# Optimization experiments

Measured on AMD Instinct MI355X. Metric: run time of the kernel, lower is better.

## Reference

```python
import jax, jax.numpy as jnp
import numpy as np

B, N, C = 32, 512, 256          # batch, proposals per scene, pooled feature dim
K = 16                          # knn neighbors
NN = B * N                      # total nodes = 16384
E = NN * K                      # total edges = 262144
L0_IN = 2 * C + 7               # EdgeConv layer-0 input (edge embedding appended)
EPS = 1e-5


def _xavier(key, fan_in, fan_out):
    s = float(np.sqrt(6.0 / (fan_in + fan_out)))
    return jax.random.uniform(key, (fan_in, fan_out), jnp.float32, -s, s)


def setup_inputs() -> dict:
    key = jax.random.key(0)
    ks = jax.random.split(key, 12)
    inp = {}
    inp["pooled_features"] = jax.random.normal(ks[0], (B, N, C), jnp.float32)
    inp["rois"] = jax.random.normal(ks[1], (B, N, 7), jnp.float32)
    inp["edge_src"] = jax.random.randint(ks[2], (E,), 0, NN)
    inp["edge_dst"] = jax.random.randint(ks[3], (E,), 0, NN)
    # global-info MLP: Linear(C+7 -> C) + BatchNorm(C) + ReLU
    inp["Wg"] = _xavier(ks[4], C + 7, C)
    inp["bg"] = jnp.zeros((C,), jnp.float32)
    inp["gg"] = jnp.ones((C,), jnp.float32)
    inp["betag"] = jnp.zeros((C,), jnp.float32)
    # EdgeConv 0: Linear(2C+7 -> C); EdgeConv 1,2: Linear(2C -> C)
    inp["W0"] = _xavier(ks[5], L0_IN, C)
    inp["b0"] = jnp.zeros((C,), jnp.float32)
    inp["g0"] = jnp.ones((C,), jnp.float32)
    inp["beta0"] = jnp.zeros((C,), jnp.float32)
    inp["W1"] = _xavier(ks[6], 2 * C, C)
    inp["b1"] = jnp.zeros((C,), jnp.float32)
    inp["g1"] = jnp.ones((C,), jnp.float32)
    inp["beta1"] = jnp.zeros((C,), jnp.float32)
    inp["W2"] = _xavier(ks[7], 2 * C, C)
    inp["b2"] = jnp.zeros((C,), jnp.float32)
    inp["g2"] = jnp.ones((C,), jnp.float32)
    inp["beta2"] = jnp.zeros((C,), jnp.float32)
    return inp


def _bn_relu(h, gamma, beta):
    # training-mode BatchNorm over the row (node/edge) dimension
    mu = jnp.mean(h, axis=0)
    var = jnp.mean(jnp.square(h - mu), axis=0)
    return jax.nn.relu((h - mu) * jax.lax.rsqrt(var + EPS) * gamma + beta)


def _edge_conv(x, src, dst, edge_attr, W, b, gamma, beta):
    x_j = x[src]          # source-node features  [E, D]
    x_i = x[dst]          # target-node features  [E, D]
    parts = [x_j - x_i, x_i]
    if edge_attr is not None:
        parts.append(edge_attr)
    m = jnp.concatenate(parts, axis=-1)          # [E, in_dim]
    h = _bn_relu(m @ W + b, gamma, beta)         # [E, C]
    out = jax.ops.segment_max(h, dst, num_segments=NN)  # scatter-max per target node
    return jnp.where(jnp.isneginf(out), 0.0, out)        # empty segments -> 0


def reference(pooled_features, rois, edge_src, edge_dst,
              Wg, bg, gg, betag,
              W0, b0, g0, beta0,
              W1, b1, g1, beta1,
              W2, b2, g2, beta2):
    boxes = rois.reshape(NN, 7)
    pf = pooled_features.reshape(NN, C)
    # global information MLP (CONCATENATED): cat(pooled, boxes) -> Linear+BN+ReLU
    x0 = _bn_relu(jnp.concatenate([pf, boxes], axis=-1) @ Wg + bg, gg, betag)
    # edge embedding: box delta from source to target
    edge_attr = boxes[edge_src] - boxes[edge_dst]
    x1 = _edge_conv(x0, edge_src, edge_dst, edge_attr, W0, b0, g0, beta0)
    x2 = _edge_conv(x1, edge_src, edge_dst, None, W1, b1, g1, beta1)
    x3 = _edge_conv(x2, edge_src, edge_dst, None, W2, b2, g2, beta2)
    return jnp.concatenate([x0, x1, x2, x3], axis=-1)  # related_features [NN, 4C]
```

## Files before the change

kernel.cpp:

```cpp
#include <hip/hip_runtime.h>
#include <hip/hip_bf16.h>
#include <hip/hip_fp16.h>
#include <math.h>
#include <stdint.h>


constexpr int NNODE = 16384;
constexpr int NEDGE = 262144;
constexpr int CD    = 256;
constexpr float EPSB = 1e-5f;

typedef __attribute__((ext_vector_type(8))) short bf16x8;
typedef __attribute__((ext_vector_type(8))) unsigned short u16x8;
typedef __attribute__((ext_vector_type(4))) float f32x4;
typedef __attribute__((ext_vector_type(4))) _Float16 h16x4;
typedef __attribute__((ext_vector_type(8))) _Float16 h16x8;

__device__ inline unsigned short bf_hi_rne(float f) {
  unsigned int u = __float_as_uint(f);
  u += 0x7fffu + ((u >> 16) & 1u);
  return (unsigned short)(u >> 16);
}

__device__ __forceinline__ void gload16(const void* g, void* l) {
  __builtin_amdgcn_global_load_lds(
      (__attribute__((address_space(1))) void*)(void*)g,
      (__attribute__((address_space(3))) void*)l, 16, 0, 0);
}

__global__ void build_wt(const float* __restrict__ W, const float* __restrict__ b,
                         unsigned short* __restrict__ Wth, unsigned short* __restrict__ Wtl,
                         int has_box) {
  int k = threadIdx.x;
  int n = blockIdx.x;
  if (k >= 288) return;
  float v = 0.0f;
  if (n < 256) {
    if (k < 256)      v = W[k * 256 + n];
    else if (k < 263) v = has_box ? W[(512 + (k - 256)) * 256 + n] : 0.0f;
  } else {
    int n2 = n - 256;
    if (k < 256)      v = W[(256 + k) * 256 + n2] - W[k * 256 + n2];
    else if (k < 263) v = has_box ? -W[(512 + (k - 256)) * 256 + n2] : 0.0f;
    else if (k == 263) v = b[n2];
  }
  unsigned short hi = bf_hi_rne(v);
  float fh = __uint_as_float((unsigned int)hi << 16);
  Wth[n * 288 + k] = hi;
  Wtl[n * 288 + k] = bf_hi_rne(v - fh);
}

__global__ void build_wtg(const float* __restrict__ Wg, const float* __restrict__ bg,
                          unsigned short* __restrict__ Wth, unsigned short* __restrict__ Wtl) {
  int k = threadIdx.x;
  int n = blockIdx.x;
  if (k >= 288) return;
  float v = 0.0f;
  if (k < 263)       v = Wg[k * 256 + n];
  else if (k == 263) v = bg[n];
  unsigned short hi = bf_hi_rne(v);
  float fh = __uint_as_float((unsigned int)hi << 16);
  Wth[n * 288 + k] = hi;
  Wtl[n * 288 + k] = bf_hi_rne(v - fh);
}

__global__ void build_boxf16(const float* __restrict__ rois,
                             unsigned short* __restrict__ hi, unsigned short* __restrict__ lo) {
  int n = blockIdx.x * 256 + threadIdx.x;
  u16x8 h8 = (u16x8)0, l8 = (u16x8)0;
#pragma unroll
  for (int j = 0; j < 8; j++) {
    float v = (j < 7) ? rois[n * 7 + j] : 1.0f;
    unsigned short h = bf_hi_rne(v);
    h8[j] = h;
    l8[j] = bf_hi_rne(v - __uint_as_float((unsigned int)h << 16));
  }
  *(u16x8*)(hi + (size_t)n * 32) = h8;
  *(u16x8*)(lo + (size_t)n * 32) = l8;
  u16x8 z = (u16x8)0;
#pragma unroll
  for (int c = 1; c < 4; c++) {
    *(u16x8*)(hi + (size_t)n * 32 + c * 8) = z;
    *(u16x8*)(lo + (size_t)n * 32 + c * 8) = z;
  }
}

__global__ void convert_split(const float* __restrict__ src,
                              unsigned short* __restrict__ hi, unsigned short* __restrict__ lo) {
  size_t i0 = ((size_t)blockIdx.x * 256 + threadIdx.x) * 8;
  float4 a = *(const float4*)(src + i0);
  float4 b = *(const float4*)(src + i0 + 4);
  float v[8] = {a.x, a.y, a.z, a.w, b.x, b.y, b.z, b.w};
  u16x8 h8, l8;
#pragma unroll
  for (int j = 0; j < 8; j++) {
    unsigned short h = bf_hi_rne(v[j]);
    h8[j] = h;
    l8[j] = bf_hi_rne(v[j] - __uint_as_float((unsigned int)h << 16));
  }
  *(u16x8*)(hi + i0) = h8;
  *(u16x8*)(lo + i0) = l8;
}

__global__ void hist_kernel(const int* __restrict__ dst, int* __restrict__ counts) {
  int e = blockIdx.x * 256 + threadIdx.x;
  atomicAdd(&counts[dst[e]], 1);
}

__global__ __launch_bounds__(1024) void scan_kernel(const int* __restrict__ counts,
                                                    int* __restrict__ offsets,
                                                    int* __restrict__ cursor) {
  __shared__ int ssum[1024];
  int t = threadIdx.x;
  int base = t * 16;
  int loc[16];
  int s = 0;
#pragma unroll
  for (int i = 0; i < 16; i++) { loc[i] = s; s += counts[base + i]; }
  ssum[t] = s;
  __syncthreads();
  for (int off = 1; off < 1024; off <<= 1) {
    int v = (t >= off) ? ssum[t - off] : 0;
    __syncthreads();
    ssum[t] += v;
    __syncthreads();
  }
  int excl = (t > 0) ? ssum[t - 1] : 0;
#pragma unroll
  for (int i = 0; i < 16; i++) {
    int o = excl + loc[i];
    offsets[base + i] = o;
    cursor[base + i]  = o;
  }
  if (t == 1023) offsets[NNODE] = excl + s;
}

__global__ void scatter_kernel(const int* __restrict__ src, const int* __restrict__ dst,
                               int* __restrict__ cursor, int* __restrict__ csr_src) {
  int e = blockIdx.x * 256 + threadIdx.x;
  int p = atomicAdd(&cursor[dst[e]], 1);
  csr_src[p] = src[e];
}

__global__ __launch_bounds__(256) void gemm_mfma(
    const unsigned short* __restrict__ Ah, const unsigned short* __restrict__ Al,
    const unsigned short* __restrict__ bxh, const unsigned short* __restrict__ bxl,
    const unsigned short* __restrict__ Wth, const unsigned short* __restrict__ Wtl,
    float* __restrict__ out, int Nw, int half_out) {
  __shared__ alignas(16) char lds[4 * 8192];
  const int tid  = threadIdx.x;
  const int lane = tid & 63;
  const int wave = tid >> 6;
  const int wm = wave >> 1, wn = wave & 1;
  const int m0 = blockIdx.x * 128;
  const int n0 = blockIdx.y * 128;
  const int srow = tid >> 2;
  const int sc8  = (tid & 3) * 8;

  f32x4 acc[4][4];
#pragma unroll
  for (int i = 0; i < 4; i++)
#pragma unroll
    for (int j = 0; j < 4; j++) acc[i][j] = (f32x4)0.0f;

  const int kblk = lane >> 4;
  for (int kt = 0; kt < 9; kt++) {
    if (kt) __syncthreads();
#pragma unroll
    for (int p = 0; p < 2; p++) {
      int row = p * 64 + srow;
      const unsigned short *gah, *gal;
      if (kt < 8) {
        size_t o = (size_t)(m0 + row) * 256 + kt * 32 + sc8;
        gah = Ah + o; gal = Al + o;
      } else {
        size_t o = (size_t)(m0 + row) * 32 + sc8;
        gah = bxh + o; gal = bxl + o;
      }
      gload16(gah, lds + p * 4096 + tid * 16);
      gload16(gal, lds + 8192 + p * 4096 + tid * 16);
      size_t wo = (size_t)(n0 + row) * 288 + kt * 32 + sc8;
      gload16(Wth + wo, lds + 16384 + p * 4096 + tid * 16);
      gload16(Wtl + wo, lds + 24576 + p * 4096 + tid * 16);
    }
    __syncthreads();

    bf16x8 ah[4], al[4];
#pragma unroll
    for (int i = 0; i < 4; i++) {
      int fm = wm * 64 + i * 16 + (lane & 15);
      int off = fm * 64 + 16 * kblk;
      ah[i] = *(const bf16x8*)(lds + off);
      al[i] = *(const bf16x8*)(lds + 8192 + off);
    }
#pragma unroll
    for (int j = 0; j < 4; j++) {
      int fn = wn * 64 + j * 16 + (lane & 15);
      int off = fn * 64 + 16 * kblk;
      bf16x8 bh = *(const bf16x8*)(lds + 16384 + off);
      bf16x8 bl = *(const bf16x8*)(lds + 24576 + off);
#pragma unroll
      for (int i = 0; i < 4; i++) {
        acc[i][j] = __builtin_amdgcn_mfma_f32_16x16x32_bf16(bh, ah[i], acc[i][j], 0, 0, 0);
        acc[i][j] = __builtin_amdgcn_mfma_f32_16x16x32_bf16(bh, al[i], acc[i][j], 0, 0, 0);
        acc[i][j] = __builtin_amdgcn_mfma_f32_16x16x32_bf16(bl, ah[i], acc[i][j], 0, 0, 0);
      }
    }
  }
#pragma unroll
  for (int i = 0; i < 4; i++) {
    int m = m0 + wm * 64 + i * 16 + (lane & 15);
#pragma unroll
    for (int j = 0; j < 4; j++) {
      int n = n0 + wn * 64 + j * 16 + (lane >> 4) * 4;
      if (half_out) {
        h16x4 o;
        o[0] = (_Float16)acc[i][j].x; o[1] = (_Float16)acc[i][j].y;
        o[2] = (_Float16)acc[i][j].z; o[3] = (_Float16)acc[i][j].w;
        *(h16x4*)((_Float16*)out + (size_t)m * Nw + n) = o;
      } else {
        *(f32x4*)(out + (size_t)m * Nw + n) = acc[i][j];
      }
    }
  }
}

constexpr int EPB = 8;
__global__ __launch_bounds__(256) void edge_pass(
    const _Float16* __restrict__ PQ,
    const int* __restrict__ offsets, const int* __restrict__ csr_src,
    float* __restrict__ M, float* __restrict__ psum, float* __restrict__ psq) {
  __shared__ float red[2][4][256];
  const int tid = threadIdx.x;
  const int wave = tid >> 6, lane = tid & 63;
  const int h = lane >> 5, li = lane & 31;
  const int c8 = li * 8;
  float sum[8] = {}, sq[8] = {};

  const int d0 = blockIdx.x * EPB + wave * 2;
  const int d1 = d0 + 1;
  int e0 = offsets[d0];
  const int end0 = offsets[d0 + 1];
  int e1 = offsets[d1];
  const int end1 = offsets[d1 + 1];

  h16x8 q0v = *(const h16x8*)(PQ + (size_t)d0 * 512 + 256 + c8);
  h16x8 q1v = *(const h16x8*)(PQ + (size_t)d1 * 512 + 256 + c8);
  float q0[8], q1[8], mx0[8], mx1[8];
#pragma unroll
  for (int j = 0; j < 8; j++) {
    q0[j] = (float)q0v[j]; q1[j] = (float)q1v[j];
    mx0[j] = -INFINITY;    mx1[j] = -INFINITY;
  }

  while (e0 < end0 || e1 < end1) {
    const bool a0 = e0 < end0, a1 = e1 < end1;
    int i0[4], i1[4];
    if (a0) {
#pragma unroll
      for (int i = 0; i < 4; i++) {
        int ei = e0 + 2 * i + h;
        i0[i] = csr_src[ei < end0 ? ei : end0 - 1];
      }
    }
    if (a1) {
#pragma unroll
      for (int i = 0; i < 4; i++) {
        int ei = e1 + 2 * i + h;
        i1[i] = csr_src[ei < end1 ? ei : end1 - 1];
      }
    }
    h16x8 p0[4], p1[4];
    if (a0) {
#pragma unroll
      for (int i = 0; i < 4; i++)
        p0[i] = *(const h16x8*)(PQ + (size_t)i0[i] * 512 + c8);
    }
    if (a1) {
#pragma unroll
      for (int i = 0; i < 4; i++)
        p1[i] = *(const h16x8*)(PQ + (size_t)i1[i] * 512 + c8);
    }

#define PROC_NODE(P, Q, MX, EE, END)                                        \
    {                                                                       \
      const int nl = (END) - (EE);                                          \
      if (nl >= 8) {                                                        \
        _Pragma("unroll")                                                   \
        for (int i = 0; i < 4; i++)                                         \
          _Pragma("unroll")                                                 \
          for (int j = 0; j < 8; j++) {                                     \
            float hh = (float)P[i][j] + Q[j];                               \
            MX[j] = fmaxf(MX[j], hh);                                       \
            sum[j] += hh; sq[j] = fmaf(hh, hh, sq[j]);                      \
          }                                                                 \
      } else {                                                              \
        _Pragma("unroll")                                                   \
        for (int i = 0; i < 4; i++) {                                       \
          const bool live = (2 * i + h) < nl;                               \
          _Pragma("unroll")                                                 \
          for (int j = 0; j < 8; j++) {                                     \
            float hh = (float)P[i][j] + Q[j];                               \
            MX[j] = fmaxf(MX[j], hh);                                       \
            float z = live ? hh : 0.f;                                      \
            sum[j] += z; sq[j] = fmaf(z, z, sq[j]);                         \
          }                                                                 \
        }                                                                   \
      }                                                                     \
    }

    if (a0) { PROC_NODE(p0, q0, mx0, e0, end0); e0 += 8; }
    if (a1) { PROC_NODE(p1, q1, mx1, e1, end1); e1 += 8; }
#undef PROC_NODE
  }

#pragma unroll
  for (int j = 0; j < 8; j++) {
    mx0[j] = fmaxf(mx0[j], __shfl_xor(mx0[j], 32));
    mx1[j] = fmaxf(mx1[j], __shfl_xor(mx1[j], 32));
  }
  float4 o0 = (h == 0) ? make_float4(mx0[0], mx0[1], mx0[2], mx0[3])
                       : make_float4(mx0[4], mx0[5], mx0[6], mx0[7]);
  float4 o1 = (h == 0) ? make_float4(mx1[0], mx1[1], mx1[2], mx1[3])
                       : make_float4(mx1[4], mx1[5], mx1[6], mx1[7]);
  *(float4*)(M + (size_t)d0 * 256 + c8 + h * 4) = o0;
  *(float4*)(M + (size_t)d1 * 256 + c8 + h * 4) = o1;

#pragma unroll
  for (int j = 0; j < 8; j++) {
    sum[j] += __shfl_xor(sum[j], 32);
    sq[j]  += __shfl_xor(sq[j], 32);
  }
  if (h == 0) {
    *(float4*)&red[0][wave][c8]     = make_float4(sum[0], sum[1], sum[2], sum[3]);
    *(float4*)&red[0][wave][c8 + 4] = make_float4(sum[4], sum[5], sum[6], sum[7]);
    *(float4*)&red[1][wave][c8]     = make_float4(sq[0], sq[1], sq[2], sq[3]);
    *(float4*)&red[1][wave][c8 + 4] = make_float4(sq[4], sq[5], sq[6], sq[7]);
  }
  __syncthreads();
  int c = tid;
  float ts = red[0][0][c] + red[0][1][c] + red[0][2][c] + red[0][3][c];
  float tq = red[1][0][c] + red[1][1][c] + red[1][2][c] + red[1][3][c];
  atomicAdd(&psum[c], ts);
  atomicAdd(&psq[c], tq);
}

__global__ void stats_dense(const float* __restrict__ H,
                            float* __restrict__ psum, float* __restrict__ psq) {
  int c  = threadIdx.x;
  int r0 = blockIdx.x * 16;
  float sum = 0.f, sq = 0.f;
  for (int r = r0; r < r0 + 16; r++) {
    float h = H[r * CD + c];
    sum += h;
    sq  += h * h;
  }
  atomicAdd(&psum[c], sum);
  atomicAdd(&psq[c], sq);
}

__global__ void finalize_stats(const float* __restrict__ psum, const float* __restrict__ psq,
                               float invcount, float* __restrict__ mu, float* __restrict__ rstd) {
  int c = threadIdx.x;
  float m = psum[c] * invcount;
  float v = psq[c] * invcount - m * m;
  v = fmaxf(v, 0.0f);
  mu[c]   = m;
  rstd[c] = 1.0f / sqrtf(v + EPSB);
}

__global__ void normalize_write(const float* __restrict__ H, const int* __restrict__ counts,
                                const float* __restrict__ mu, const float* __restrict__ rstd,
                                const float* __restrict__ gamma, const float* __restrict__ beta,
                                float* __restrict__ out, int col0,
                                unsigned short* __restrict__ xh, unsigned short* __restrict__ xl) {
  int c  = threadIdx.x;
  int n0 = blockIdx.x * 8;
  float mc = mu[c], rc = rstd[c], gc = gamma[c], bc = beta[c];
  for (int n = n0; n < n0 + 8; n++) {
    float v = 0.0f;
    if (!counts || counts[n] != 0) {
      float h = H[n * CD + c];
      v = fmaxf((h - mc) * rc * gc + bc, 0.0f);
    }
    out[n * 1024 + col0 + c] = v;
    if (xh) {
      unsigned short hv = bf_hi_rne(v);
      xh[(size_t)n * 256 + c] = hv;
      xl[(size_t)n * 256 + c] = bf_hi_rne(v - __uint_as_float((unsigned int)hv << 16));
    }
  }
}

extern "C" void kernel_launch(void* const* d_in, const int* in_sizes, int n_in,
                              void* d_out, int out_size, void* d_ws, size_t ws_size,
                              hipStream_t stream) {
  const float* pf    = (const float*)d_in[0];
  const float* rois  = (const float*)d_in[1];
  const int*   esrc  = (const int*)d_in[2];
  const int*   edst  = (const int*)d_in[3];
  const float* Wg    = (const float*)d_in[4];
  const float* bg    = (const float*)d_in[5];
  const float* gg    = (const float*)d_in[6];
  const float* betag = (const float*)d_in[7];
  const float* Wl[3]  = {(const float*)d_in[8],  (const float*)d_in[12], (const float*)d_in[16]};
  const float* bl[3]  = {(const float*)d_in[9],  (const float*)d_in[13], (const float*)d_in[17]};
  const float* gl[3]  = {(const float*)d_in[10], (const float*)d_in[14], (const float*)d_in[18]};
  const float* bel[3] = {(const float*)d_in[11], (const float*)d_in[15], (const float*)d_in[19]};
  float* out = (float*)d_out;

  float* ws    = (float*)d_ws;
  _Float16* PQ = (_Float16*)ws;
  float* Mbuf  = ws + (size_t)NNODE * 256;
  float* psum  = Mbuf + (size_t)NNODE * CD;
  float* psq   = psum + CD;
  float* mu    = psq + CD;
  float* rstd  = mu + CD;
  unsigned short* Ah = (unsigned short*)(rstd + CD);
  unsigned short* Al = Ah + (size_t)NNODE * 256;
  unsigned short* bxh = Al + (size_t)NNODE * 256;
  unsigned short* bxl = bxh + (size_t)NNODE * 32;
  unsigned short* wt  = bxl + (size_t)NNODE * 32;
  unsigned short* wtg_h = wt + 3 * 2 * 512 * 288;
  unsigned short* wtg_l = wtg_h + 256 * 288;
  int* counts  = (int*)(wtg_l + 256 * 288);
  int* offsets = counts + NNODE;
  int* cursor  = offsets + NNODE + 1;
  int* csr     = cursor + NNODE;

  hipMemsetAsync(counts, 0, NNODE * sizeof(int), stream);
  build_boxf16<<<NNODE / 256, 256, 0, stream>>>(rois, bxh, bxl);
  convert_split<<<NNODE * CD / (256 * 8), 256, 0, stream>>>(pf, Ah, Al);
  build_wtg<<<256, 320, 0, stream>>>(Wg, bg, wtg_h, wtg_l);
  for (int l = 0; l < 3; l++)
    build_wt<<<512, 320, 0, stream>>>(Wl[l], bl[l],
                                      wt + l * 2 * 512 * 288,
                                      wt + l * 2 * 512 * 288 + 512 * 288,
                                      l == 0 ? 1 : 0);
  hist_kernel<<<NEDGE / 256, 256, 0, stream>>>(edst, counts);
  scan_kernel<<<1, 1024, 0, stream>>>(counts, offsets, cursor);
  scatter_kernel<<<NEDGE / 256, 256, 0, stream>>>(esrc, edst, cursor, csr);

  hipMemsetAsync(psum, 0, 2 * CD * sizeof(float), stream);
  {
    dim3 g(NNODE / 128, 2);
    gemm_mfma<<<g, 256, 0, stream>>>(Ah, Al, bxh, bxl, wtg_h, wtg_l, Mbuf, 256, 0);
  }
  stats_dense<<<NNODE / 16, 256, 0, stream>>>(Mbuf, psum, psq);
  finalize_stats<<<1, 256, 0, stream>>>(psum, psq, 1.0f / NNODE, mu, rstd);
  normalize_write<<<NNODE / 8, 256, 0, stream>>>(Mbuf, nullptr, mu, rstd, gg, betag,
                                                 out, 0, Ah, Al);

  for (int l = 0; l < 3; l++) {
    dim3 g(NNODE / 128, 4);
    gemm_mfma<<<g, 256, 0, stream>>>(Ah, Al, bxh, bxl,
                                     wt + l * 2 * 512 * 288,
                                     wt + l * 2 * 512 * 288 + 512 * 288,
                                     (float*)PQ, 512, 1);
    hipMemsetAsync(psum, 0, 2 * CD * sizeof(float), stream);
    edge_pass<<<NNODE / EPB, 256, 0, stream>>>(PQ, offsets, csr, Mbuf, psum, psq);
    finalize_stats<<<1, 256, 0, stream>>>(psum, psq, 1.0f / NEDGE, mu, rstd);
    normalize_write<<<NNODE / 8, 256, 0, stream>>>(Mbuf, counts, mu, rstd, gl[l], bel[l],
                                                   out, (l + 1) * CD,
                                                   l < 2 ? Ah : nullptr,
                                                   l < 2 ? Al : nullptr);
  }
}
```

Measured before the change: 495.2 us.

## Drop split-bf16 error compensation and restructure edge pass with fp16 packed math

Removes the hi/lo bf16 split for activations, boxes and weights, so each GEMM issues one MFMA per tile instead of three and loads half as much data into half the LDS. The edge pass now assigns one destination node per wave in 512-thread blocks, double-buffers the neighbour gathers, skips empty nodes, and computes add and max in packed fp16. Accuracy drops to plain bf16 GEMM inputs and fp16 intermediate sums, which may breach the tolerance against the fp32 reference.

```diff
diff --git a/kernel.cpp b/kernel.cpp
--- a/kernel.cpp
+++ b/kernel.cpp
@@ -15,6 +15,7 @@
 typedef __attribute__((ext_vector_type(4))) float f32x4;
 typedef __attribute__((ext_vector_type(4))) _Float16 h16x4;
 typedef __attribute__((ext_vector_type(8))) _Float16 h16x8;
+typedef __attribute__((ext_vector_type(2))) _Float16 h16x2;
 
 __device__ inline unsigned short bf_hi_rne(float f) {
   unsigned int u = __float_as_uint(f);
@@ -29,8 +30,7 @@
 }
 
 __global__ void build_wt(const float* __restrict__ W, const float* __restrict__ b,
-                         unsigned short* __restrict__ Wth, unsigned short* __restrict__ Wtl,
-                         int has_box) {
+                         unsigned short* __restrict__ Wth, int has_box) {
   int k = threadIdx.x;
   int n = blockIdx.x;
   if (k >= 288) return;
@@ -44,62 +44,45 @@
     else if (k < 263) v = has_box ? -W[(512 + (k - 256)) * 256 + n2] : 0.0f;
     else if (k == 263) v = b[n2];
   }
-  unsigned short hi = bf_hi_rne(v);
-  float fh = __uint_as_float((unsigned int)hi << 16);
-  Wth[n * 288 + k] = hi;
-  Wtl[n * 288 + k] = bf_hi_rne(v - fh);
+  Wth[n * 288 + k] = bf_hi_rne(v);
 }
 
 __global__ void build_wtg(const float* __restrict__ Wg, const float* __restrict__ bg,
-                          unsigned short* __restrict__ Wth, unsigned short* __restrict__ Wtl) {
+                          unsigned short* __restrict__ Wth) {
   int k = threadIdx.x;
   int n = blockIdx.x;
   if (k >= 288) return;
   float v = 0.0f;
   if (k < 263)       v = Wg[k * 256 + n];
   else if (k == 263) v = bg[n];
-  unsigned short hi = bf_hi_rne(v);
-  float fh = __uint_as_float((unsigned int)hi << 16);
-  Wth[n * 288 + k] = hi;
-  Wtl[n * 288 + k] = bf_hi_rne(v - fh);
+  Wth[n * 288 + k] = bf_hi_rne(v);
 }
 
 __global__ void build_boxf16(const float* __restrict__ rois,
-                             unsigned short* __restrict__ hi, unsigned short* __restrict__ lo) {
+                             unsigned short* __restrict__ hi) {
   int n = blockIdx.x * 256 + threadIdx.x;
-  u16x8 h8 = (u16x8)0, l8 = (u16x8)0;
+  u16x8 h8 = (u16x8)0;
 #pragma unroll
   for (int j = 0; j < 8; j++) {
     float v = (j < 7) ? rois[n * 7 + j] : 1.0f;
-    unsigned short h = bf_hi_rne(v);
-    h8[j] = h;
-    l8[j] = bf_hi_rne(v - __uint_as_float((unsigned int)h << 16));
+    h8[j] = bf_hi_rne(v);
   }
   *(u16x8*)(hi + (size_t)n * 32) = h8;
-  *(u16x8*)(lo + (size_t)n * 32) = l8;
   u16x8 z = (u16x8)0;
 #pragma unroll
-  for (int c = 1; c < 4; c++) {
-    *(u16x8*)(hi + (size_t)n * 32 + c * 8) = z;
-    *(u16x8*)(lo + (size_t)n * 32 + c * 8) = z;
-  }
+  for (int c = 1; c < 4; c++) *(u16x8*)(hi + (size_t)n * 32 + c * 8) = z;
 }
 
 __global__ void convert_split(const float* __restrict__ src,
-                              unsigned short* __restrict__ hi, unsigned short* __restrict__ lo) {
+                              unsigned short* __restrict__ hi) {
   size_t i0 = ((size_t)blockIdx.x * 256 + threadIdx.x) * 8;
   float4 a = *(const float4*)(src + i0);
   float4 b = *(const float4*)(src + i0 + 4);
   float v[8] = {a.x, a.y, a.z, a.w, b.x, b.y, b.z, b.w};
-  u16x8 h8, l8;
-#pragma unroll
-  for (int j = 0; j < 8; j++) {
-    unsigned short h = bf_hi_rne(v[j]);
-    h8[j] = h;
-    l8[j] = bf_hi_rne(v[j] - __uint_as_float((unsigned int)h << 16));
-  }
+  u16x8 h8;
+#pragma unroll
+  for (int j = 0; j < 8; j++) h8[j] = bf_hi_rne(v[j]);
   *(u16x8*)(hi + i0) = h8;
-  *(u16x8*)(lo + i0) = l8;
 }
 
 __global__ void hist_kernel(const int* __restrict__ dst, int* __restrict__ counts) {
@@ -143,11 +126,11 @@
 }
 
 __global__ __launch_bounds__(256) void gemm_mfma(
-    const unsigned short* __restrict__ Ah, const unsigned short* __restrict__ Al,
-    const unsigned short* __restrict__ bxh, const unsigned short* __restrict__ bxl,
-    const unsigned short* __restrict__ Wth, const unsigned short* __restrict__ Wtl,
+    const unsigned short* __restrict__ Ah,
+    const unsigned short* __restrict__ bxh,
+    const unsigned short* __restrict__ Wth,
     float* __restrict__ out, int Nw, int half_out) {
-  __shared__ alignas(16) char lds[4 * 8192];
+  __shared__ alignas(16) char lds[2 * 8192];
   const int tid  = threadIdx.x;
   const int lane = tid & 63;
   const int wave = tid >> 6;
@@ -169,42 +152,28 @@
 #pragma unroll
     for (int p = 0; p < 2; p++) {
       int row = p * 64 + srow;
-      const unsigned short *gah, *gal;
-      if (kt < 8) {
-        size_t o = (size_t)(m0 + row) * 256 + kt * 32 + sc8;
-        gah = Ah + o; gal = Al + o;
-      } else {
-        size_t o = (size_t)(m0 + row) * 32 + sc8;
-        gah = bxh + o; gal = bxl + o;
-      }
-      gload16(gah, lds + p * 4096 + tid * 16);
-      gload16(gal, lds + 8192 + p * 4096 + tid * 16);
-      size_t wo = (size_t)(n0 + row) * 288 + kt * 32 + sc8;
-      gload16(Wth + wo, lds + 16384 + p * 4096 + tid * 16);
-      gload16(Wtl + wo, lds + 24576 + p * 4096 + tid * 16);
+      const unsigned short* ga =
+          (kt < 8) ? Ah + (size_t)(m0 + row) * 256 + kt * 32 + sc8
+                   : bxh + (size_t)(m0 + row) * 32 + sc8;
+      gload16(ga, lds + p * 4096 + tid * 16);
+      gload16(Wth + (size_t)(n0 + row) * 288 + kt * 32 + sc8,
+              lds + 8192 + p * 4096 + tid * 16);
     }
     __syncthreads();
 
-    bf16x8 ah[4], al[4];
+    bf16x8 ah[4];
 #pragma unroll
     for (int i = 0; i < 4; i++) {
       int fm = wm * 64 + i * 16 + (lane & 15);
-      int off = fm * 64 + 16 * kblk;
-      ah[i] = *(const bf16x8*)(lds + off);
-      al[i] = *(const bf16x8*)(lds + 8192 + off);
+      ah[i] = *(const bf16x8*)(lds + fm * 64 + 16 * kblk);
     }
 #pragma unroll
     for (int j = 0; j < 4; j++) {
       int fn = wn * 64 + j * 16 + (lane & 15);
-      int off = fn * 64 + 16 * kblk;
-      bf16x8 bh = *(const bf16x8*)(lds + 16384 + off);
-      bf16x8 bl = *(const bf16x8*)(lds + 24576 + off);
-#pragma unroll
-      for (int i = 0; i < 4; i++) {
+      bf16x8 bh = *(const bf16x8*)(lds + 8192 + fn * 64 + 16 * kblk);
+#pragma unroll
+      for (int i = 0; i < 4; i++)
         acc[i][j] = __builtin_amdgcn_mfma_f32_16x16x32_bf16(bh, ah[i], acc[i][j], 0, 0, 0);
-        acc[i][j] = __builtin_amdgcn_mfma_f32_16x16x32_bf16(bh, al[i], acc[i][j], 0, 0, 0);
-        acc[i][j] = __builtin_amdgcn_mfma_f32_16x16x32_bf16(bl, ah[i], acc[i][j], 0, 0, 0);
-      }
     }
   }
 #pragma unroll
@@ -225,106 +194,103 @@
   }
 }
 
-constexpr int EPB = 8;
-__global__ __launch_bounds__(256) void edge_pass(
+__global__ __launch_bounds__(512) void edge_pass(
     const _Float16* __restrict__ PQ,
     const int* __restrict__ offsets, const int* __restrict__ csr_src,
     float* __restrict__ M, float* __restrict__ psum, float* __restrict__ psq) {
-  __shared__ float red[2][4][256];
+  __shared__ float red[2][8][256];
   const int tid = threadIdx.x;
   const int wave = tid >> 6, lane = tid & 63;
   const int h = lane >> 5, li = lane & 31;
   const int c8 = li * 8;
   float sum[8] = {}, sq[8] = {};
 
-  const int d0 = blockIdx.x * EPB + wave * 2;
-  const int d1 = d0 + 1;
-  int e0 = offsets[d0];
-  const int end0 = offsets[d0 + 1];
-  int e1 = offsets[d1];
-  const int end1 = offsets[d1 + 1];
-
-  h16x8 q0v = *(const h16x8*)(PQ + (size_t)d0 * 512 + 256 + c8);
-  h16x8 q1v = *(const h16x8*)(PQ + (size_t)d1 * 512 + 256 + c8);
-  float q0[8], q1[8], mx0[8], mx1[8];
-#pragma unroll
-  for (int j = 0; j < 8; j++) {
-    q0[j] = (float)q0v[j]; q1[j] = (float)q1v[j];
-    mx0[j] = -INFINITY;    mx1[j] = -INFINITY;
-  }
-
-  while (e0 < end0 || e1 < end1) {
-    const bool a0 = e0 < end0, a1 = e1 < end1;
-    int i0[4], i1[4];
-    if (a0) {
-#pragma unroll
-      for (int i = 0; i < 4; i++) {
-        int ei = e0 + 2 * i + h;
-        i0[i] = csr_src[ei < end0 ? ei : end0 - 1];
-      }
-    }
-    if (a1) {
-#pragma unroll
-      for (int i = 0; i < 4; i++) {
-        int ei = e1 + 2 * i + h;
-        i1[i] = csr_src[ei < end1 ? ei : end1 - 1];
-      }
-    }
-    h16x8 p0[4], p1[4];
-    if (a0) {
-#pragma unroll
-      for (int i = 0; i < 4; i++)
-        p0[i] = *(const h16x8*)(PQ + (size_t)i0[i] * 512 + c8);
-    }
-    if (a1) {
-#pragma unroll
-      for (int i = 0; i < 4; i++)
-        p1[i] = *(const h16x8*)(PQ + (size_t)i1[i] * 512 + c8);
-    }
-
-#define PROC_NODE(P, Q, MX, EE, END)                                        \
-    {                                                                       \
-      const int nl = (END) - (EE);                                          \
-      if (nl >= 8) {                                                        \
-        _Pragma("unroll")                                                   \
-        for (int i = 0; i < 4; i++)                                         \
-          _Pragma("unroll")                                                 \
-          for (int j = 0; j < 8; j++) {                                     \
-            float hh = (float)P[i][j] + Q[j];                               \
-            MX[j] = fmaxf(MX[j], hh);                                       \
-            sum[j] += hh; sq[j] = fmaf(hh, hh, sq[j]);                      \
-          }                                                                 \
-      } else {                                                              \
-        _Pragma("unroll")                                                   \
-        for (int i = 0; i < 4; i++) {                                       \
-          const bool live = (2 * i + h) < nl;                               \
-          _Pragma("unroll")                                                 \
-          for (int j = 0; j < 8; j++) {                                     \
-            float hh = (float)P[i][j] + Q[j];                               \
-            MX[j] = fmaxf(MX[j], hh);                                       \
-            float z = live ? hh : 0.f;                                      \
-            sum[j] += z; sq[j] = fmaf(z, z, sq[j]);                         \
-          }                                                                 \
-        }                                                                   \
-      }                                                                     \
-    }
-
-    if (a0) { PROC_NODE(p0, q0, mx0, e0, end0); e0 += 8; }
-    if (a1) { PROC_NODE(p1, q1, mx1, e1, end1); e1 += 8; }
-#undef PROC_NODE
-  }
-
-#pragma unroll
-  for (int j = 0; j < 8; j++) {
-    mx0[j] = fmaxf(mx0[j], __shfl_xor(mx0[j], 32));
-    mx1[j] = fmaxf(mx1[j], __shfl_xor(mx1[j], 32));
-  }
-  float4 o0 = (h == 0) ? make_float4(mx0[0], mx0[1], mx0[2], mx0[3])
-                       : make_float4(mx0[4], mx0[5], mx0[6], mx0[7]);
-  float4 o1 = (h == 0) ? make_float4(mx1[0], mx1[1], mx1[2], mx1[3])
-                       : make_float4(mx1[4], mx1[5], mx1[6], mx1[7]);
-  *(float4*)(M + (size_t)d0 * 256 + c8 + h * 4) = o0;
-  *(float4*)(M + (size_t)d1 * 256 + c8 + h * 4) = o1;
+  const int d = blockIdx.x * 8 + wave;
+  const int beg = offsets[d], end = offsets[d + 1];
+  const bool any = beg < end;
+
+  if (any) {
+    h16x8 qv = *(const h16x8*)(PQ + (size_t)d * 512 + 256 + c8);
+    h16x2 q2[4], mx2[4];
+    _Float16 NINF = (_Float16)(-INFINITY);
+#pragma unroll
+    for (int jj = 0; jj < 4; jj++) {
+      q2[jj][0] = qv[2 * jj]; q2[jj][1] = qv[2 * jj + 1];
+      mx2[jj][0] = NINF;      mx2[jj][1] = NINF;
+    }
+
+#define LOADIDX(I, E)                                                     \
+    _Pragma("unroll") for (int i = 0; i < 4; i++) {                       \
+      int ei = (E) + 2 * i + h;                                           \
+      I[i] = csr_src[ei < end ? ei : end - 1];           \
+    }
+#define GATHER(P, I)                                                      \
+    _Pragma("unroll") for (int i = 0; i < 4; i++)                         \
+      P[i] = *(const h16x8*)(PQ + (size_t)I[i] * 512 + c8);
+#define PROC(P, E)                                                        \
+    {                                                                     \
+      const int nl = end - (E);                                           \
+      if (nl >= 8) {                                                      \
+        _Pragma("unroll") for (int i = 0; i < 4; i++)                     \
+          _Pragma("unroll") for (int jj = 0; jj < 4; jj++) {              \
+            h16x2 pp; pp[0] = P[i][2 * jj]; pp[1] = P[i][2 * jj + 1];     \
+            h16x2 hh = pp + q2[jj];                     \
+            mx2[jj] = __builtin_elementwise_max(mx2[jj], hh);             \
+            float h0 = (float)hh[0], h1 = (float)hh[1];                   \
+            sum[2 * jj] += h0; sum[2 * jj + 1] += h1;                     \
+            sq[2 * jj] = fmaf(h0, h0, sq[2 * jj]);                        \
+            sq[2 * jj + 1] = fmaf(h1, h1, sq[2 * jj + 1]);                \
+          }                                                               \
+      } else {                                                            \
+        _Pragma("unroll") for (int i = 0; i < 4; i++) {                   \
+          const bool live = (2 * i + h) < nl;                             \
+          _Pragma("unroll") for (int jj = 0; jj < 4; jj++) {              \
+            h16x2 pp; pp[0] = P[i][2 * jj]; pp[1] = P[i][2 * jj + 1];     \
+            h16x2 hh = pp + q2[jj];                                       \
+            mx2[jj] = __builtin_elementwise_max(mx2[jj], hh);             \
+            float h0 = (float)hh[0], h1 = (float)hh[1];                   \
+            float z0 = live ? h0 : 0.f, z1 = live ? h1 : 0.f;             \
+            sum[2 * jj] += z0; sum[2 * jj + 1] += z1;                     \
+            sq[2 * jj] = fmaf(z0, z0, sq[2 * jj]);                        \
+            sq[2 * jj + 1] = fmaf(z1, z1, sq[2 * jj + 1]);                \
+          }                                                               \
+        }                                                                 \
+      }                                                                   \
+    }
+
+    int iA[4], iB[4];
+    h16x8 pA[4], pB[4];
+    LOADIDX(iA, beg);
+    GATHER(pA, iA);
+    if (beg + 8 < end) { LOADIDX(iB, beg + 8); GATHER(pB, iB); }
+    int e = beg;
+    while (true) {
+      PROC(pA, e);
+      if (e + 16 < end) { LOADIDX(iA, e + 16); GATHER(pA, iA); }
+      e += 8;
+      if (e >= end) break;
+      PROC(pB, e);
+      if (e + 16 < end) { LOADIDX(iB, e + 16); GATHER(pB, iB); }
+      e += 8;
+      if (e >= end) break;
+    }
+#undef LOADIDX
+#undef GATHER
+#undef PROC
+
+    float mxf[8];
+#pragma unroll
+    for (int jj = 0; jj < 4; jj++) {
+      mxf[2 * jj]     = (float)mx2[jj][0];
+      mxf[2 * jj + 1] = (float)mx2[jj][1];
+    }
+#pragma unroll
+    for (int j = 0; j < 8; j++)
+      mxf[j] = fmaxf(mxf[j], __shfl_xor(mxf[j], 32));
+    float4 o = (h == 0) ? make_float4(mxf[0], mxf[1], mxf[2], mxf[3])
+                        : make_float4(mxf[4], mxf[5], mxf[6], mxf[7]);
+    *(float4*)(M + (size_t)d * 256 + c8 + h * 4) = o;
+  }
 
 #pragma unroll
   for (int j = 0; j < 8; j++) {
@@ -338,11 +304,13 @@
     *(float4*)&red[1][wave][c8 + 4] = make_float4(sq[4], sq[5], sq[6], sq[7]);
   }
   __syncthreads();
-  int c = tid;
-  float ts = red[0][0][c] + red[0][1][c] + red[0][2][c] + red[0][3][c];
-  float tq = red[1][0][c] + red[1][1][c] + red[1][2][c] + red[1][3][c];
-  atomicAdd(&psum[c], ts);
-  atomicAdd(&psq[c], tq);
+  if (tid < 256) {
+    float ts = 0.f, tq = 0.f;
+#pragma unroll
+    for (int w = 0; w < 8; w++) { ts += red[0][w][tid]; tq += red[1][w][tid]; }
+    atomicAdd(&psum[tid], ts);
+    atomicAdd(&psq[tid], tq);
+  }
 }
 
 __global__ void stats_dense(const float* __restrict__ H,
@@ -373,7 +341,7 @@
                                 const float* __restrict__ mu, const float* __restrict__ rstd,
                                 const float* __restrict__ gamma, const float* __restrict__ beta,
                                 float* __restrict__ out, int col0,
-                                unsigned short* __restrict__ xh, unsigned short* __restrict__ xl) {
+                                unsigned short* __restrict__ xh) {
   int c  = threadIdx.x;
   int n0 = blockIdx.x * 8;
   float mc = mu[c], rc = rstd[c], gc = gamma[c], bc = beta[c];
@@ -384,11 +352,7 @@
       v = fmaxf((h - mc) * rc * gc + bc, 0.0f);
     }
     out[n * 1024 + col0 + c] = v;
-    if (xh) {
-      unsigned short hv = bf_hi_rne(v);
-      xh[(size_t)n * 256 + c] = hv;
-      xl[(size_t)n * 256 + c] = bf_hi_rne(v - __uint_as_float((unsigned int)hv << 16));
-    }
+    if (xh) xh[(size_t)n * 256 + c] = bf_hi_rne(v);
   }
 }
 
@@ -416,27 +380,21 @@
   float* psq   = psum + CD;
   float* mu    = psq + CD;
   float* rstd  = mu + CD;
-  unsigned short* Ah = (unsigned short*)(rstd + CD);
-  unsigned short* Al = Ah + (size_t)NNODE * 256;
-  unsigned short* bxh = Al + (size_t)NNODE * 256;
-  unsigned short* bxl = bxh + (size_t)NNODE * 32;
-  unsigned short* wt  = bxl + (size_t)NNODE * 32;
-  unsigned short* wtg_h = wt + 3 * 2 * 512 * 288;
-  unsigned short* wtg_l = wtg_h + 256 * 288;
-  int* counts  = (int*)(wtg_l + 256 * 288);
+  unsigned short* Ah  = (unsigned short*)(rstd + CD);
+  unsigned short* bxh = Ah + (size_t)NNODE * 256;
+  unsigned short* wt  = bxh + (size_t)NNODE * 32;
+  unsigned short* wtg = wt + 3 * 512 * 288;
+  int* counts  = (int*)(wtg + 256 * 288);
   int* offsets = counts + NNODE;
   int* cursor  = offsets + NNODE + 1;
   int* csr     = cursor + NNODE;
 
   hipMemsetAsync(counts, 0, NNODE * sizeof(int), stream);
-  build_boxf16<<<NNODE / 256, 256, 0, stream>>>(rois, bxh, bxl);
-  convert_split<<<NNODE * CD / (256 * 8), 256, 0, stream>>>(pf, Ah, Al);
-  build_wtg<<<256, 320, 0, stream>>>(Wg, bg, wtg_h, wtg_l);
+  build_boxf16<<<NNODE / 256, 256, 0, stream>>>(rois, bxh);
+  convert_split<<<NNODE * CD / (256 * 8), 256, 0, stream>>>(pf, Ah);
+  build_wtg<<<256, 320, 0, stream>>>(Wg, bg, wtg);
   for (int l = 0; l < 3; l++)
-    build_wt<<<512, 320, 0, stream>>>(Wl[l], bl[l],
-                                      wt + l * 2 * 512 * 288,
-                                      wt + l * 2 * 512 * 288 + 512 * 288,
-                                      l == 0 ? 1 : 0);
+    build_wt<<<512, 320, 0, stream>>>(Wl[l], bl[l], wt + l * 512 * 288, l == 0 ? 1 : 0);
   hist_kernel<<<NEDGE / 256, 256, 0, stream>>>(edst, counts);
   scan_kernel<<<1, 1024, 0, stream>>>(counts, offsets, cursor);
   scatter_kernel<<<NEDGE / 256, 256, 0, stream>>>(esrc, edst, cursor, csr);
@@ -444,25 +402,21 @@
   hipMemsetAsync(psum, 0, 2 * CD * sizeof(float), stream);
   {
     dim3 g(NNODE / 128, 2);
-    gemm_mfma<<<g, 256, 0, stream>>>(Ah, Al, bxh, bxl, wtg_h, wtg_l, Mbuf, 256, 0);
+    gemm_mfma<<<g, 256, 0, stream>>>(Ah, bxh, wtg, Mbuf, 256, 0);
   }
   stats_dense<<<NNODE / 16, 256, 0, stream>>>(Mbuf, psum, psq);
   finalize_stats<<<1, 256, 0, stream>>>(psum, psq, 1.0f / NNODE, mu, rstd);
   normalize_write<<<NNODE / 8, 256, 0, stream>>>(Mbuf, nullptr, mu, rstd, gg, betag,
-                                                 out, 0, Ah, Al);
+                                                 out, 0, Ah);
 
   for (int l = 0; l < 3; l++) {
     dim3 g(NNODE / 128, 4);
-    gemm_mfma<<<g, 256, 0, stream>>>(Ah, Al, bxh, bxl,
-                                     wt + l * 2 * 512 * 288,
-                                     wt + l * 2 * 512 * 288 + 512 * 288,
-                                     (float*)PQ, 512, 1);
+    gemm_mfma<<<g, 256, 0, stream>>>(Ah, bxh, wt + l * 512 * 288, (float*)PQ, 512, 1);
     hipMemsetAsync(psum, 0, 2 * CD * sizeof(float), stream);
-    edge_pass<<<NNODE / EPB, 256, 0, stream>>>(PQ, offsets, csr, Mbuf, psum, psq);
+    edge_pass<<<NNODE / 8, 512, 0, stream>>>(PQ, offsets, csr, Mbuf, psum, psq);
     finalize_stats<<<1, 256, 0, stream>>>(psum, psq, 1.0f / NEDGE, mu, rstd);
     normalize_write<<<NNODE / 8, 256, 0, stream>>>(Mbuf, counts, mu, rstd, gl[l], bel[l],
                                                    out, (l + 1) * CD,
-                                                   l < 2 ? Ah : nullptr,
-                                                   l < 2 ? Al : nullptr);
-  }
-}
+                                                   l < 2 ? Ah : nullptr);
+  }
+}
```

Result: faster. 460.4 us (-7.0%).
